# Kernel tuning notes

Hardware: AMD Instinct MI355X
Metric: run time of the kernel (lower is better)

## Reference

```python
import jax, jax.numpy as jnp
import numpy as np

_SAMPLING_EPS = 1e-5
BIG_NEG = jnp.float32(-1e30)  # finite stand-in for -inf (exact 0 after softmax in fp32)


def setup_inputs() -> dict:
    key = jax.random.key(0)
    ks = jax.random.split(key, 12)
    B, V, P, O, S = 128, 128000, 2048, 256, 4
    return {
        "logits": jax.random.normal(ks[0], (B, V), jnp.float32) * 4.0,
        "prompt_token_ids": jax.random.randint(ks[1], (B, P), 0, V),
        "output_token_ids": jax.random.randint(ks[2], (B, O), 0, V),
        "stop_token_ids": jax.random.randint(ks[3], (B, S), 0, V),
        "min_tokens": jax.random.randint(ks[4], (B,), 0, 512),
        "presence_penalties": jax.random.uniform(ks[5], (B,), jnp.float32),
        "frequency_penalties": jax.random.uniform(ks[6], (B,), jnp.float32),
        "repetition_penalties": 1.0 + 0.3 * jax.random.uniform(ks[7], (B,), jnp.float32),
        "temperature": 0.5 + jax.random.uniform(ks[8], (B,), jnp.float32),
        "top_k": jax.random.randint(ks[9], (B,), 32, 64),
        "top_p": 0.5 + 0.5 * jax.random.uniform(ks[10], (B,), jnp.float32),
        "uniform_noise": jax.random.uniform(ks[11], (B, V), jnp.float32, minval=1e-10, maxval=1.0),
        "max_num_logprobs": 20,
    }


def reference(logits, prompt_token_ids, output_token_ids, stop_token_ids,
              min_tokens, presence_penalties, frequency_penalties,
              repetition_penalties, temperature, top_k, top_p,
              uniform_noise, max_num_logprobs):
    B, V = logits.shape
    x = logits.astype(jnp.float32)
    rows = jnp.arange(B)[:, None]

    # ---- min-token penalty: set stop-token logits to -inf while len(output) < min_tokens
    need = min_tokens > output_token_ids.shape[1]                  # [B]
    stop_pen = jnp.where(need[:, None], BIG_NEG, jnp.inf)          # [B,S]
    x = x.at[rows, stop_token_ids].min(stop_pen)

    # ---- presence / frequency / repetition penalties (vLLM apply_penalties)
    counts = jnp.zeros((B, V), jnp.float32).at[rows, output_token_ids].add(1.0)
    prompt_mask = jnp.zeros((B, V), bool).at[rows, prompt_token_ids].set(True)
    output_mask = counts > 0
    rp = repetition_penalties[:, None]
    penalized = jnp.where(x > 0, x / rp, x * rp)
    x = jnp.where(prompt_mask | output_mask, penalized, x)
    x = x - frequency_penalties[:, None] * counts \
          - presence_penalties[:, None] * output_mask.astype(jnp.float32)

    # ---- temperature (greedy rows: temp treated as 1.0)
    t = jnp.where(temperature < _SAMPLING_EPS, 1.0, temperature)
    x = x / t[:, None]

    # ---- top-k / top-p filtering (per-row k and p)
    order = jnp.argsort(-x, axis=-1)                               # descending
    srt = jnp.take_along_axis(x, order, axis=-1)
    pos = jnp.arange(V)[None, :]
    k_eff = jnp.where(top_k < 1, V, top_k)
    keep_k = pos < k_eff[:, None]
    probs_s = jax.nn.softmax(srt, axis=-1)
    cum = jnp.cumsum(probs_s, axis=-1)
    keep_p = (cum - probs_s) < top_p[:, None]                      # cumulative mass before token < p
    keep = jnp.zeros((B, V), bool).at[rows, order].set(keep_k & keep_p)
    x = jnp.where(keep, x, BIG_NEG)

    orig_logits = x
    # source applies temperature a second time before the final sample
    x2 = x / t[:, None]

    # ---- sample: Gumbel-max random sampling, greedy where temperature ~ 0
    gumbel = -jnp.log(-jnp.log(uniform_noise))
    random_sampled = jnp.argmax(x2 + gumbel, axis=-1)
    greedy_sampled = jnp.argmax(x2, axis=-1)
    sampled = jnp.where(temperature < _SAMPLING_EPS, greedy_sampled,
                        random_sampled).astype(jnp.int32)

    # ---- top-k logprobs
    logprobs = jax.nn.log_softmax(orig_logits, axis=-1)
    topk_logprobs, topk_indices = jax.lax.top_k(logprobs, max_num_logprobs)
    return sampled, topk_logprobs, topk_indices.astype(jnp.int32)
```

## Files before the change

kernel.cpp:

```cpp
#include <hip/hip_runtime.h>
#include <math.h>

#define VV 128000
#define NB 128
#define PP 2048
#define OO 256
#define GW 4000

#define S   8
#define CH  16000
#define CW  500
#define NT0 512
#define NT1 512
#define CAP 512
#define HS1 512

#define NT2 256

#define BIG_NEG_F (-1e30f)
#define PAD_KEY 0x007FFFFF80000000ULL
#define LOG2E 1.4426950408889634f

__device__ __forceinline__ unsigned long long packkey(float f, int idx) {
  unsigned int b = __float_as_uint(f);
  unsigned int mf = (b & 0x80000000u) ? ~b : (b | 0x80000000u);
  return ((unsigned long long)mf << 32) | (unsigned long long)(unsigned int)(~(unsigned int)idx);
}
__device__ __forceinline__ float unpack_val(unsigned long long k) {
  unsigned int mf = (unsigned int)(k >> 32);
  unsigned int b = (mf & 0x80000000u) ? (mf & 0x7fffffffu) : ~mf;
  return __uint_as_float(b);
}
__device__ __forceinline__ int unpack_idx(unsigned long long k) {
  return (int)(~(unsigned int)(k & 0xffffffffu));
}
__device__ __forceinline__ float ulp_down(float f, int n) {
  unsigned int b = __float_as_uint(f);
  unsigned int m = (b & 0x80000000u) ? ~b : (b | 0x80000000u);
  m -= (unsigned int)n;
  unsigned int r = (m & 0x80000000u) ? (m & 0x7fffffffu) : ~m;
  return __uint_as_float(r);
}

__device__ __forceinline__ float wave_sort64_desc(float v, int lane) {
  for (int k = 2; k <= 64; k <<= 1) {
    for (int j = k >> 1; j > 0; j >>= 1) {
      float o = __shfl_xor(v, j, 64);
      bool smaller = (lane & j) == 0;
      bool dir = (lane & k) == 0;
      v = (smaller == dir) ? fmaxf(v, o) : fminf(v, o);
    }
  }
  return v;
}
__device__ __forceinline__ unsigned long long wave_sort64_desc_u64(unsigned long long v, int lane) {
  for (int k = 2; k <= 64; k <<= 1) {
    for (int j = k >> 1; j > 0; j >>= 1) {
      unsigned long long o = __shfl_xor(v, j, 64);
      bool smaller = (lane & j) == 0;
      bool dir = (lane & k) == 0;
      unsigned long long mx = (v > o) ? v : o;
      unsigned long long mn = (v > o) ? o : v;
      v = (smaller == dir) ? mx : mn;
    }
  }
  return v;
}
__device__ __forceinline__ unsigned long long merge_top64(unsigned long long v,
                                                          const unsigned long long* B,
                                                          int lane) {
  unsigned long long b = B[63 - lane];
  v = (v > b) ? v : b;
  for (int j = 32; j > 0; j >>= 1) {
    unsigned long long o = __shfl_xor(v, j, 64);
    bool hi = (lane & j) == 0;
    unsigned long long mx = (v > o) ? v : o;
    unsigned long long mn = (v > o) ? o : v;
    v = hi ? mx : mn;
  }
  return v;
}

__global__ __launch_bounds__(NT0)
void k0_build(const int* __restrict__ prompt_ids,
              const int* __restrict__ output_ids,
              unsigned int* __restrict__ ws_pb,
              unsigned int* __restrict__ ws_ob,
              int* __restrict__ ws_hk,
              int* __restrict__ ws_hv)
{
  __shared__ int hkey[HS1];
  __shared__ int hval[HS1];
  const int row = blockIdx.x;
  const int tid = threadIdx.x;

  unsigned int* pb = ws_pb + (size_t)row * GW;
  unsigned int* ob = ws_ob + (size_t)row * GW;
  uint4* pb4 = (uint4*)pb;
  uint4* ob4 = (uint4*)ob;
  uint4 z; z.x = 0u; z.y = 0u; z.z = 0u; z.w = 0u;
  for (int i = tid; i < GW / 4; i += NT0) { pb4[i] = z; ob4[i] = z; }
  for (int i = tid; i < HS1; i += NT0) { hkey[i] = -1; hval[i] = 0; }
  __syncthreads();

  const int4* pr4 = (const int4*)(prompt_ids + (size_t)row * PP);
  for (int i = tid; i < PP / 4; i += NT0) {
    int4 tv = pr4[i];
    atomicOr(&pb[tv.x >> 5], 1u << (tv.x & 31));
    atomicOr(&pb[tv.y >> 5], 1u << (tv.y & 31));
    atomicOr(&pb[tv.z >> 5], 1u << (tv.z & 31));
    atomicOr(&pb[tv.w >> 5], 1u << (tv.w & 31));
  }
  for (int i = tid; i < OO; i += NT0) {
    int tok = output_ids[row * OO + i];
    atomicOr(&ob[tok >> 5], 1u << (tok & 31));
    unsigned int h = ((unsigned int)tok * 2654435761u) >> 23;
    for (;;) {
      int k = hkey[h];
      if (k == tok) { atomicAdd(&hval[h], 1); break; }
      if (k == -1) {
        int prev = atomicCAS(&hkey[h], -1, tok);
        if (prev == -1 || prev == tok) { atomicAdd(&hval[h], 1); break; }
        continue;
      }
      h = (h + 1) & (HS1 - 1);
    }
  }
  __syncthreads();
  for (int i = tid; i < HS1; i += NT0) {
    ws_hk[row * HS1 + i] = hkey[i];
    ws_hv[row * HS1 + i] = hval[i];
  }
}

__global__ __launch_bounds__(NT1)
void k1_select(const float* __restrict__ logits,
               const int* __restrict__ stop_ids,
               const int* __restrict__ min_tokens,
               const float* __restrict__ presence_p,
               const float* __restrict__ frequency_p,
               const float* __restrict__ repetition_p,
               const float* __restrict__ temperature,
               const unsigned int* __restrict__ ws_pb,
               const unsigned int* __restrict__ ws_ob,
               const int* __restrict__ ws_hk,
               const int* __restrict__ ws_hv,
               unsigned long long* __restrict__ ws_top,
               float* __restrict__ ws_sum)
{
#pragma clang fp contract(off)
  __shared__ unsigned int pbits[CW];
  __shared__ unsigned int obits[CW];
  __shared__ int hkey[HS1];
  __shared__ int hval[HS1];
  __shared__ unsigned long long cand[CAP];
  __shared__ unsigned long long mbuf[4 * 64];
  __shared__ float wtau[NT1 / 64];
  __shared__ float wsum[NT1 / 64];
  __shared__ float tau_sh;
  __shared__ int cnt_sh;

  const int chunk = blockIdx.x;
  const int row   = blockIdx.y;
  const int tid   = threadIdx.x;
  const int lane  = tid & 63;
  const int wv    = tid >> 6;
  const int base  = chunk * CH;

  const float fp  = frequency_p[row];
  const float pp  = presence_p[row];
  const float rp  = repetition_p[row];
  const float inv_rp = 1.0f / rp;
  const float tmp = temperature[row];
  const float t   = (tmp < 1e-5f) ? 1.0f : tmp;
  const float c2  = LOG2E / t;
  const bool need = min_tokens[row] > OO;
  const int s0 = stop_ids[row * 4 + 0];
  const int s1 = stop_ids[row * 4 + 1];
  const int s2 = stop_ids[row * 4 + 2];
  const int s3 = stop_ids[row * 4 + 3];
  const bool anystop = need &&
      (((unsigned)(s0 - base) < CH) || ((unsigned)(s1 - base) < CH) ||
       ((unsigned)(s2 - base) < CH) || ((unsigned)(s3 - base) < CH));

  const unsigned int* pbg = ws_pb + (size_t)row * GW + chunk * CW;
  const unsigned int* obg = ws_ob + (size_t)row * GW + chunk * CW;
  for (int i = tid; i < CW; i += NT1) { pbits[i] = pbg[i]; obits[i] = obg[i]; }
  for (int i = tid; i < HS1; i += NT1) {
    hkey[i] = ws_hk[row * HS1 + i];
    hval[i] = ws_hv[row * HS1 + i];
  }
  if (tid == 0) cnt_sh = 0;
  __syncthreads();

  const float* __restrict__ lrow = logits + (size_t)row * VV + base;
  const int l0 = (0 * NT1 + tid) << 3;
  const int l1 = (1 * NT1 + tid) << 3;
  const int l2 = (2 * NT1 + tid) << 3;
  const int l3 = (3 * NT1 + tid) << 3;
  const bool v3 = l3 < CH;

  unsigned int stopmask = 0u;
  if (anystop) {
    const int sids[4] = {s0, s1, s2, s3};
#pragma unroll
    for (int q = 0; q < 4; ++q) {
      int local = sids[q] - base;
      if ((unsigned)local < CH) {
        int grp = (local >> 3) / NT1;
        int tt  = (local >> 3) % NT1;
        if (tt == tid) stopmask |= 1u << (grp * 8 + (local & 7));
      }
    }
  }

  float4 A0 = *(const float4*)(lrow + l0);
  float4 B0 = *(const float4*)(lrow + l0 + 4);
  float4 A1 = *(const float4*)(lrow + l1);
  float4 B1 = *(const float4*)(lrow + l1 + 4);
  float4 A2 = *(const float4*)(lrow + l2);
  float4 B2 = *(const float4*)(lrow + l2 + 4);
  float4 A3, B3;
  if (v3) { A3 = *(const float4*)(lrow + l3); B3 = *(const float4*)(lrow + l3 + 4); }

  float gm0 = -INFINITY, gm1 = -INFINITY, gm2 = -INFINITY, gm3 = -INFINITY;
  float esum = 0.0f;

  auto processA = [&](int li, float4 xa, float4 xb, float& gm, unsigned int sm8) {
    unsigned int w  = (unsigned)li >> 5;
    unsigned int sh = (unsigned)li & 31u;
    unsigned int pm8 = (pbits[w] >> sh) & 255u;
    unsigned int om8 = (obits[w] >> sh) & 255u;
    float xs[8] = {xa.x, xa.y, xa.z, xa.w, xb.x, xb.y, xb.z, xb.w};
    if (sm8) {
#pragma unroll
      for (int e = 0; e < 8; ++e)
        if ((sm8 >> e) & 1u) xs[e] = BIG_NEG_F;
    }
#pragma unroll
    for (int e = 0; e < 8; ++e) {
      float xp = xs[e];
      if ((pm8 | om8) & (1u << e)) {
        xp = (xp > 0.0f) ? (xp * inv_rp) : (xp * rp);
        if ((om8 >> e) & 1u) {
          int v = base + li + e;
          float cnt = 0.0f;
          unsigned int h = ((unsigned int)v * 2654435761u) >> 23;
          for (;;) {
            int k = hkey[h];
            if (k == -1) break;
            if (k == v) { cnt = (float)hval[h]; break; }
            h = (h + 1) & (HS1 - 1);
          }
          xp = xp - fp * cnt - pp;
        }
      }
      gm = fmaxf(gm, xp);
      esum += exp2f(xp * c2);
    }
  };

  processA(l0, A0, B0, gm0, stopmask & 255u);
  processA(l1, A1, B1, gm1, (stopmask >> 8) & 255u);
  processA(l2, A2, B2, gm2, (stopmask >> 16) & 255u);
  if (v3) processA(l3, A3, B3, gm3, (stopmask >> 24) & 255u);

  float mx = fmaxf(fmaxf(gm0, gm1), fmaxf(gm2, gm3));

  float ss = esum;
#pragma unroll
  for (int off = 32; off > 0; off >>= 1) ss += __shfl_down(ss, off, 64);
  if (lane == 0) wsum[wv] = ss;

  float srt = wave_sort64_desc(mx, lane);
  if (lane == 7) wtau[wv] = srt;
  __syncthreads();

  if (tid == 0) {
    float tau = wtau[0];
#pragma unroll
    for (int w = 1; w < NT1 / 64; ++w) tau = fminf(tau, wtau[w]);
    tau_sh = ulp_down(tau, 16);
    float sacc = 0.0f;
#pragma unroll
    for (int w = 0; w < NT1 / 64; ++w) sacc += wsum[w];
    ws_sum[row * S + chunk] = sacc;
  }
  __syncthreads();
  const float taueff = tau_sh;

  auto processB = [&](int li, float gmv) {
    if (gmv < taueff) return;
    float4 xa = *(const float4*)(lrow + li);
    float4 xb = *(const float4*)(lrow + li + 4);
    float xs[8] = {xa.x, xa.y, xa.z, xa.w, xb.x, xb.y, xb.z, xb.w};
#pragma unroll
    for (int e = 0; e < 8; ++e) {
      float x = xs[e];
      if (x >= taueff) {
        int v = base + li + e;
        int ll = li + e;
        if (anystop && ((v == s0) | (v == s1) | (v == s2) | (v == s3)))
          x = fminf(x, BIG_NEG_F);
        bool pm = (pbits[(unsigned)ll >> 5] >> ((unsigned)ll & 31u)) & 1u;
        bool om = (obits[(unsigned)ll >> 5] >> ((unsigned)ll & 31u)) & 1u;
        float cnt = 0.0f;
        if (om) {
          unsigned int h = ((unsigned int)v * 2654435761u) >> 23;
          for (;;) {
            int k = hkey[h];
            if (k == -1) break;
            if (k == v) { cnt = (float)hval[h]; break; }
            h = (h + 1) & (HS1 - 1);
          }
        }
        if (pm || om) x = (x > 0.0f) ? (x / rp) : (x * rp);
        x = x - fp * cnt;
        if (om) x = x - pp;
        if (x >= taueff) {
          float xd = x / t;
          int p = atomicAdd(&cnt_sh, 1);
          if (p < CAP) cand[p] = packkey(xd, v);
        }
      }
    }
  };

  processB(l0, gm0);
  processB(l1, gm1);
  processB(l2, gm2);
  if (v3) processB(l3, gm3);

  __syncthreads();
  int total = cnt_sh; if (total > CAP) total = CAP;
  for (int i = tid; i < CAP; i += NT1)
    if (i >= total) cand[i] = PAD_KEY;
  __syncthreads();

  unsigned long long rv = wave_sort64_desc_u64(cand[(wv << 6) + lane], lane);
  cand[(wv << 6) + lane] = rv;
  __syncthreads();

  if (wv < 4) {
    unsigned long long a = cand[((2 * wv) << 6) + lane];
    a = merge_top64(a, &cand[(2 * wv + 1) << 6], lane);
    mbuf[(wv << 6) + lane] = a;
  }
  __syncthreads();
  if (wv < 2) {
    unsigned long long a = mbuf[((2 * wv) << 6) + lane];
    a = merge_top64(a, &mbuf[(2 * wv + 1) << 6], lane);
    cand[(wv << 6) + lane] = a;
  }
  __syncthreads();
  if (wv == 0) {
    unsigned long long a = cand[lane];
    a = merge_top64(a, &cand[64], lane);
    ws_top[((size_t)row * S + chunk) * 64 + lane] = a;
  }
}

__global__ __launch_bounds__(NT2)
void k2_finalize(const float* __restrict__ temperature,
                 const int* __restrict__ top_k,
                 const float* __restrict__ top_p,
                 const float* __restrict__ noise,
                 const unsigned long long* __restrict__ ws_top,
                 const float* __restrict__ ws_sum,
                 float* __restrict__ out, int K)
{
#pragma clang fp contract(off)
  __shared__ unsigned long long buf[S * 64];
  __shared__ unsigned long long mbuf[4 * 64];
  __shared__ float sv[64];
  __shared__ int   si[64];
  __shared__ float se[64];
  __shared__ float gv[64];

  const int row  = blockIdx.x;
  const int tid  = threadIdx.x;
  const int lane = tid & 63;
  const int wv   = tid >> 6;

  const float tmp = temperature[row];
  const float t   = (tmp < 1e-5f) ? 1.0f : tmp;
  const int   tk  = top_k[row];
  const float tpv = top_p[row];

  for (int i = tid; i < S * 64; i += NT2)
    buf[i] = ws_top[(size_t)row * S * 64 + i];
  __syncthreads();

  {
    unsigned long long a = buf[((2 * wv) << 6) + lane];
    a = merge_top64(a, &buf[(2 * wv + 1) << 6], lane);
    mbuf[(wv << 6) + lane] = a;
  }
  __syncthreads();
  if (wv < 2) {
    unsigned long long a = mbuf[((2 * wv) << 6) + lane];
    a = merge_top64(a, &mbuf[(2 * wv + 1) << 6], lane);
    buf[(wv << 6) + lane] = a;
  }
  __syncthreads();
  if (wv == 0) {
    unsigned long long a = buf[lane];
    a = merge_top64(a, &buf[64], lane);
    float val = unpack_val(a);
    int   idx = unpack_idx(a);
    float m = __shfl(val, 0, 64);
    sv[lane] = val;
    si[lane] = idx;
    bool ok = (unsigned)idx < VV;
    float u = ok ? noise[(size_t)row * VV + idx] : 0.5f;
    float g = -logf(-logf(u));
    se[lane] = expf(val - m);
    gv[lane] = val / t + g;
  }
  __syncthreads();

  if (tid == 0) {
    float Ssum = 0.0f;
    for (int c = 0; c < S; c++) Ssum += ws_sum[row * S + c];
    const float m = sv[0];
    const float Z = Ssum * exp2f(-m * LOG2E);

    int keff = (tk < 1) ? 64 : (tk < 64 ? tk : 64);

    float cum = 0.0f;
    int nk = 0;
    for (int j = 0; j < 64; j++) {
      if (j >= keff) break;
      if (!(cum < tpv)) break;
      nk++;
      cum += se[j] / Z;
    }

    float Zk = 0.0f;
    for (int j = 0; j < nk; j++) Zk += se[j];
    const float logZk = logf(Zk);

    float bv = -INFINITY; int bi = 0x7fffffff;
    for (int j = 0; j < nk; j++) {
      float val = gv[j];
      if (val > bv || (val == bv && si[j] < bi)) { bv = val; bi = si[j]; }
    }
    const int samp = (tmp < 1e-5f) ? si[0] : bi;
    out[row] = (float)samp;

    unsigned long long bm0 = 0ull, bm1 = 0ull;
    for (int j = 0; j < nk; j++) {
      int ix = si[j];
      if (ix < 64) bm0 |= 1ull << ix;
      else if (ix < 128) bm1 |= 1ull << (ix - 64);
    }
    int fi = 0;
    for (int j = 0; j < K; j++) {
      float lp; int ix;
      if (j < nk) {
        lp = (sv[j] - m) - logZk;
        ix = si[j];
      } else {
        while ((fi < 64) ? ((bm0 >> fi) & 1ull) : ((bm1 >> (fi - 64)) & 1ull)) fi++;
        ix = fi; fi++;
        lp = BIG_NEG_F;
      }
      out[NB + row * K + j]            = lp;
      out[NB + NB * K + row * K + j]   = (float)ix;
    }
  }
}

extern "C" void kernel_launch(void* const* d_in, const int* in_sizes, int n_in,
                              void* d_out, int out_size, void* d_ws, size_t ws_size,
                              hipStream_t stream) {
  const float* logits = (const float*)d_in[0];
  const int*   prompt = (const int*)d_in[1];
  const int*   outids = (const int*)d_in[2];
  const int*   stop   = (const int*)d_in[3];
  const int*   mint   = (const int*)d_in[4];
  const float* pres   = (const float*)d_in[5];
  const float* freq   = (const float*)d_in[6];
  const float* rep    = (const float*)d_in[7];
  const float* temp   = (const float*)d_in[8];
  const int*   topk   = (const int*)d_in[9];
  const float* topp   = (const float*)d_in[10];
  const float* noise  = (const float*)d_in[11];

  int B_ = in_sizes[4];
  int K_ = (out_size - B_) / (2 * B_);

  unsigned long long* ws_top = (unsigned long long*)d_ws;
  unsigned int* ws_pb = (unsigned int*)(ws_top + (size_t)NB * S * 64);
  unsigned int* ws_ob = ws_pb + (size_t)NB * GW;
  int* ws_hk = (int*)(ws_ob + (size_t)NB * GW);
  int* ws_hv = ws_hk + (size_t)NB * HS1;
  float* ws_sum = (float*)(ws_hv + (size_t)NB * HS1);

  k0_build<<<B_, NT0, 0, stream>>>(prompt, outids, ws_pb, ws_ob, ws_hk, ws_hv);
  dim3 g1(S, B_);
  k1_select<<<g1, NT1, 0, stream>>>(logits, stop, mint, pres, freq, rep, temp,
                                    ws_pb, ws_ob, ws_hk, ws_hv,
                                    ws_top, ws_sum);
  k2_finalize<<<B_, NT2, 0, stream>>>(temp, topk, topp, noise,
                                      ws_top, ws_sum, (float*)d_out, K_);
}
```

Before: 209.3 us.

## Fuse build, select and finalize into one kernel with last-block finalize

Drops the separate bitmap/hash-build kernel: each chunk block now builds its own prompt/output bitmaps and count hash in shared memory by scanning the row's full prompt and output token lists and keeping only tokens in its chunk. The finalize stage becomes a last-block-done step guarded by an atomic counter and thread fences, replacing the third kernel. This removes two launches and the global workspace round trip, but each of the 8 chunk blocks rescans all 2048 prompt ids, and a memset is added to reset the counters.

```diff
diff --git a/kernel.cpp b/kernel.cpp
--- a/kernel.cpp
+++ b/kernel.cpp
@@ -5,17 +5,13 @@
 #define NB 128
 #define PP 2048
 #define OO 256
-#define GW 4000
 
 #define S   8
 #define CH  16000
 #define CW  500
-#define NT0 512
 #define NT1 512
 #define CAP 512
 #define HS1 512
-
-#define NT2 256
 
 #define BIG_NEG_F (-1e30f)
 #define PAD_KEY 0x007FFFFF80000000ULL
@@ -81,72 +77,23 @@
   return v;
 }
 
-__global__ __launch_bounds__(NT0)
-void k0_build(const int* __restrict__ prompt_ids,
-              const int* __restrict__ output_ids,
-              unsigned int* __restrict__ ws_pb,
-              unsigned int* __restrict__ ws_ob,
-              int* __restrict__ ws_hk,
-              int* __restrict__ ws_hv)
-{
-  __shared__ int hkey[HS1];
-  __shared__ int hval[HS1];
-  const int row = blockIdx.x;
-  const int tid = threadIdx.x;
-
-  unsigned int* pb = ws_pb + (size_t)row * GW;
-  unsigned int* ob = ws_ob + (size_t)row * GW;
-  uint4* pb4 = (uint4*)pb;
-  uint4* ob4 = (uint4*)ob;
-  uint4 z; z.x = 0u; z.y = 0u; z.z = 0u; z.w = 0u;
-  for (int i = tid; i < GW / 4; i += NT0) { pb4[i] = z; ob4[i] = z; }
-  for (int i = tid; i < HS1; i += NT0) { hkey[i] = -1; hval[i] = 0; }
-  __syncthreads();
-
-  const int4* pr4 = (const int4*)(prompt_ids + (size_t)row * PP);
-  for (int i = tid; i < PP / 4; i += NT0) {
-    int4 tv = pr4[i];
-    atomicOr(&pb[tv.x >> 5], 1u << (tv.x & 31));
-    atomicOr(&pb[tv.y >> 5], 1u << (tv.y & 31));
-    atomicOr(&pb[tv.z >> 5], 1u << (tv.z & 31));
-    atomicOr(&pb[tv.w >> 5], 1u << (tv.w & 31));
-  }
-  for (int i = tid; i < OO; i += NT0) {
-    int tok = output_ids[row * OO + i];
-    atomicOr(&ob[tok >> 5], 1u << (tok & 31));
-    unsigned int h = ((unsigned int)tok * 2654435761u) >> 23;
-    for (;;) {
-      int k = hkey[h];
-      if (k == tok) { atomicAdd(&hval[h], 1); break; }
-      if (k == -1) {
-        int prev = atomicCAS(&hkey[h], -1, tok);
-        if (prev == -1 || prev == tok) { atomicAdd(&hval[h], 1); break; }
-        continue;
-      }
-      h = (h + 1) & (HS1 - 1);
-    }
-  }
-  __syncthreads();
-  for (int i = tid; i < HS1; i += NT0) {
-    ws_hk[row * HS1 + i] = hkey[i];
-    ws_hv[row * HS1 + i] = hval[i];
-  }
-}
-
 __global__ __launch_bounds__(NT1)
-void k1_select(const float* __restrict__ logits,
-               const int* __restrict__ stop_ids,
-               const int* __restrict__ min_tokens,
-               const float* __restrict__ presence_p,
-               const float* __restrict__ frequency_p,
-               const float* __restrict__ repetition_p,
-               const float* __restrict__ temperature,
-               const unsigned int* __restrict__ ws_pb,
-               const unsigned int* __restrict__ ws_ob,
-               const int* __restrict__ ws_hk,
-               const int* __restrict__ ws_hv,
-               unsigned long long* __restrict__ ws_top,
-               float* __restrict__ ws_sum)
+void k_all(const float* __restrict__ logits,
+           const int* __restrict__ prompt_ids,
+           const int* __restrict__ output_ids,
+           const int* __restrict__ stop_ids,
+           const int* __restrict__ min_tokens,
+           const float* __restrict__ presence_p,
+           const float* __restrict__ frequency_p,
+           const float* __restrict__ repetition_p,
+           const float* __restrict__ temperature,
+           const int* __restrict__ top_k,
+           const float* __restrict__ top_p,
+           const float* __restrict__ noise,
+           int* __restrict__ ws_cnt,
+           float* __restrict__ ws_sum,
+           unsigned long long* __restrict__ ws_top,
+           float* __restrict__ out, int K)
 {
 #pragma clang fp contract(off)
   __shared__ unsigned int pbits[CW];
@@ -159,6 +106,11 @@
   __shared__ float wsum[NT1 / 64];
   __shared__ float tau_sh;
   __shared__ int cnt_sh;
+  __shared__ int last_sh;
+  __shared__ float sv[64];
+  __shared__ int   si[64];
+  __shared__ float se[64];
+  __shared__ float gv[64];
 
   const int chunk = blockIdx.x;
   const int row   = blockIdx.y;
@@ -183,14 +135,38 @@
       (((unsigned)(s0 - base) < CH) || ((unsigned)(s1 - base) < CH) ||
        ((unsigned)(s2 - base) < CH) || ((unsigned)(s3 - base) < CH));
 
-  const unsigned int* pbg = ws_pb + (size_t)row * GW + chunk * CW;
-  const unsigned int* obg = ws_ob + (size_t)row * GW + chunk * CW;
-  for (int i = tid; i < CW; i += NT1) { pbits[i] = pbg[i]; obits[i] = obg[i]; }
-  for (int i = tid; i < HS1; i += NT1) {
-    hkey[i] = ws_hk[row * HS1 + i];
-    hval[i] = ws_hv[row * HS1 + i];
-  }
+  for (int i = tid; i < CW; i += NT1) { pbits[i] = 0u; obits[i] = 0u; }
+  for (int i = tid; i < HS1; i += NT1) { hkey[i] = -1; hval[i] = 0; }
   if (tid == 0) cnt_sh = 0;
+  __syncthreads();
+
+  const int4* pr4 = (const int4*)(prompt_ids + (size_t)row * PP);
+  for (int i = tid; i < PP / 4; i += NT1) {
+    int4 tv = pr4[i];
+    int l;
+    l = tv.x - base; if ((unsigned)l < CH) atomicOr(&pbits[l >> 5], 1u << (l & 31));
+    l = tv.y - base; if ((unsigned)l < CH) atomicOr(&pbits[l >> 5], 1u << (l & 31));
+    l = tv.z - base; if ((unsigned)l < CH) atomicOr(&pbits[l >> 5], 1u << (l & 31));
+    l = tv.w - base; if ((unsigned)l < CH) atomicOr(&pbits[l >> 5], 1u << (l & 31));
+  }
+  for (int i = tid; i < OO; i += NT1) {
+    int tok = output_ids[row * OO + i];
+    int l = tok - base;
+    if ((unsigned)l < CH) {
+      atomicOr(&obits[l >> 5], 1u << (l & 31));
+      unsigned int h = ((unsigned int)tok * 2654435761u) >> 23;
+      for (;;) {
+        int k = hkey[h];
+        if (k == tok) { atomicAdd(&hval[h], 1); break; }
+        if (k == -1) {
+          int prev = atomicCAS(&hkey[h], -1, tok);
+          if (prev == -1 || prev == tok) { atomicAdd(&hval[h], 1); break; }
+          continue;
+        }
+        h = (h + 1) & (HS1 - 1);
+      }
+    }
+  }
   __syncthreads();
 
   const float* __restrict__ lrow = logits + (size_t)row * VV + base;
@@ -358,54 +334,38 @@
     a = merge_top64(a, &cand[64], lane);
     ws_top[((size_t)row * S + chunk) * 64 + lane] = a;
   }
-}
-
-__global__ __launch_bounds__(NT2)
-void k2_finalize(const float* __restrict__ temperature,
-                 const int* __restrict__ top_k,
-                 const float* __restrict__ top_p,
-                 const float* __restrict__ noise,
-                 const unsigned long long* __restrict__ ws_top,
-                 const float* __restrict__ ws_sum,
-                 float* __restrict__ out, int K)
-{
-#pragma clang fp contract(off)
-  __shared__ unsigned long long buf[S * 64];
-  __shared__ unsigned long long mbuf[4 * 64];
-  __shared__ float sv[64];
-  __shared__ int   si[64];
-  __shared__ float se[64];
-  __shared__ float gv[64];
-
-  const int row  = blockIdx.x;
-  const int tid  = threadIdx.x;
-  const int lane = tid & 63;
-  const int wv   = tid >> 6;
-
-  const float tmp = temperature[row];
-  const float t   = (tmp < 1e-5f) ? 1.0f : tmp;
-  const int   tk  = top_k[row];
+
+  __threadfence();
+  __syncthreads();
+  if (tid == 0) last_sh = (atomicAdd(&ws_cnt[row], 1) == S - 1);
+  __syncthreads();
+  if (!last_sh) return;
+  __threadfence();
+
+  const int tk  = top_k[row];
   const float tpv = top_p[row];
 
-  for (int i = tid; i < S * 64; i += NT2)
-    buf[i] = ws_top[(size_t)row * S * 64 + i];
+  for (int i = tid; i < S * 64; i += NT1)
+    cand[i] = ws_top[(size_t)row * S * 64 + i];
   __syncthreads();
 
   {
-    unsigned long long a = buf[((2 * wv) << 6) + lane];
-    a = merge_top64(a, &buf[(2 * wv + 1) << 6], lane);
-    mbuf[(wv << 6) + lane] = a;
+    if (wv < 4) {
+      unsigned long long a = cand[((2 * wv) << 6) + lane];
+      a = merge_top64(a, &cand[(2 * wv + 1) << 6], lane);
+      mbuf[(wv << 6) + lane] = a;
+    }
   }
   __syncthreads();
   if (wv < 2) {
     unsigned long long a = mbuf[((2 * wv) << 6) + lane];
     a = merge_top64(a, &mbuf[(2 * wv + 1) << 6], lane);
-    buf[(wv << 6) + lane] = a;
+    cand[(wv << 6) + lane] = a;
   }
   __syncthreads();
   if (wv == 0) {
-    unsigned long long a = buf[lane];
-    a = merge_top64(a, &buf[64], lane);
+    unsigned long long a = cand[lane];
+    a = merge_top64(a, &cand[64], lane);
     float val = unpack_val(a);
     int   idx = unpack_idx(a);
     float m = __shfl(val, 0, 64);
@@ -490,18 +450,13 @@
   int B_ = in_sizes[4];
   int K_ = (out_size - B_) / (2 * B_);
 
-  unsigned long long* ws_top = (unsigned long long*)d_ws;
-  unsigned int* ws_pb = (unsigned int*)(ws_top + (size_t)NB * S * 64);
-  unsigned int* ws_ob = ws_pb + (size_t)NB * GW;
-  int* ws_hk = (int*)(ws_ob + (size_t)NB * GW);
-  int* ws_hv = ws_hk + (size_t)NB * HS1;
-  float* ws_sum = (float*)(ws_hv + (size_t)NB * HS1);
-
-  k0_build<<<B_, NT0, 0, stream>>>(prompt, outids, ws_pb, ws_ob, ws_hk, ws_hv);
+  int* ws_cnt = (int*)d_ws;
+  float* ws_sum = (float*)(ws_cnt + NB);
+  unsigned long long* ws_top = (unsigned long long*)(ws_sum + (size_t)NB * S);
+
+  hipMemsetAsync(ws_cnt, 0, NB * sizeof(int), stream);
   dim3 g1(S, B_);
-  k1_select<<<g1, NT1, 0, stream>>>(logits, stop, mint, pres, freq, rep, temp,
-                                    ws_pb, ws_ob, ws_hk, ws_hv,
-                                    ws_top, ws_sum);
-  k2_finalize<<<B_, NT2, 0, stream>>>(temp, topk, topp, noise,
-                                      ws_top, ws_sum, (float*)d_out, K_);
-}
+  k_all<<<g1, NT1, 0, stream>>>(logits, prompt, outids, stop, mint,
+                                pres, freq, rep, temp, topk, topp, noise,
+                                ws_cnt, ws_sum, ws_top, (float*)d_out, K_);
+}
```

Measured after the change: 425.6 us. 2.03x slower.
